# Kernel tuning notes

Measured on AMD Instinct MI355X. Metric: run time of the kernel, lower is better.

The kernel has to match this reference:

```python
import jax, jax.numpy as jnp
import numpy as np

B, T, N, D, H = 4, 8, 128, 256, 8
DH = D // H
SH_HID = 16
NUM_FEATS = 3
NUM_COEFF = 4  # l=0 (1) + l=1 (3)
Y0_CONST = 0.28209479177387814   # 1/(2*sqrt(pi)), e3nn 'integral' norm
Y1_CONST = 0.4886025119029199    # sqrt(3/(4*pi))


def setup_inputs() -> dict:
    key = jax.random.key(0)
    ks = jax.random.split(key, 16)
    rn = lambda k, shape, s=1.0: jax.random.normal(k, shape, dtype=jnp.float32) * s
    return {
        "x_0": rn(ks[0], (B, T, N, D)),
        "v_0": rn(ks[1], (B, T, N, D)),
        "concatenated_features": rn(ks[2], (B, T, N, D)),
        "q_data": rn(ks[3], (B, T, N, D)),
        "mask": jnp.ones((B, 1, N, 1), dtype=bool),
        "Wq": rn(ks[4], (D, D), 0.02), "bq": jnp.zeros((D,), jnp.float32),
        "Wkv": rn(ks[5], (NUM_FEATS, D, 2 * D), 0.02),
        "bkv": jnp.zeros((NUM_FEATS, 2 * D), jnp.float32),
        "Wo": rn(ks[6], (D, D), 0.02), "bo": jnp.zeros((D,), jnp.float32),
        "feature_weights": rn(ks[7], (NUM_FEATS,), 0.1),
        "attention_denom": jnp.full((H,), float(DH), dtype=jnp.float32),
        "sh_W1": rn(ks[8], (NUM_COEFF, SH_HID), 0.3), "sh_b1": jnp.zeros((SH_HID,), jnp.float32),
        "sh_W2": rn(ks[9], (SH_HID, SH_HID), 0.3), "sh_b2": jnp.zeros((SH_HID,), jnp.float32),
        "sh_W3": rn(ks[10], (SH_HID, H), 0.3), "sh_b3": jnp.zeros((H,), jnp.float32),
    }


def _rope(t, mask, T_, N_):
    # t: [B,H,S,dh]; time-only RoPE, groups of N_ nodes share a timestep. offset=0.
    B_, H_, S, dh = t.shape
    half = dh // 2
    freqs = 1.0 / (1000.0 ** (2.0 * jnp.arange(half, dtype=jnp.float32) / dh))  # [half]
    pos = jnp.repeat(jnp.arange(T_, dtype=jnp.float32), N_)  # [S]
    angle = pos[:, None] * freqs[None, :]  # [S, half]
    mask_seq = jnp.broadcast_to(mask, (B_, T_, N_, 1)).reshape(B_, 1, S, 1)
    cos_t = jnp.where(mask_seq, jnp.cos(angle)[None, None], 1.0)  # [B,1,S,half]
    sin_t = jnp.where(mask_seq, jnp.sin(angle)[None, None], 0.0)
    t1, t2 = t[..., 0::2], t[..., 1::2]
    return jnp.stack([t1 * cos_t - t2 * sin_t, t1 * sin_t + t2 * cos_t], axis=-1).reshape(t.shape)


def _sh_bias(coords, W1, b1, W2, b2, W3, b3):
    # coords: [B,S,3] -> bias [B,H,S,S]
    rel = coords[:, :, None, :] - coords[:, None, :, :]  # [B,S,S,3]
    norm = jnp.sqrt(jnp.sum(rel * rel, axis=-1, keepdims=True))
    u = rel / (norm + 1e-6)
    Y0 = jnp.full(u.shape[:-1] + (1,), Y0_CONST, dtype=u.dtype)
    Y1 = Y1_CONST * u[..., jnp.array([1, 2, 0])]  # e3nn l=1 order (y,z,x)
    sh = jnp.concatenate([Y0, Y1], axis=-1)  # [B,S,S,4]
    h = jax.nn.silu(sh @ W1 + b1)
    h = jax.nn.silu(h @ W2 + b2)
    bias = h @ W3 + b3  # [B,S,S,H]
    return jnp.transpose(bias, (0, 3, 1, 2))


def reference(x_0, v_0, concatenated_features, q_data, mask,
              Wq, bq, Wkv, bkv, Wo, bo, feature_weights, attention_denom,
              sh_W1, sh_b1, sh_W2, sh_b2, sh_W3, sh_b3):
    B_, T_, N_, D_ = q_data.shape
    S = T_ * N_
    H_ = attention_denom.shape[0]
    dh = D_ // H_

    q = (q_data.reshape(B_, S, D_) @ Wq + bq).reshape(B_, S, H_, dh).transpose(0, 2, 1, 3)
    q = _rope(q, mask, T_, N_)

    coords = x_0[..., :3].reshape(B_, S, 3)
    bias = _sh_bias(coords, sh_W1, sh_b1, sh_W2, sh_b2, sh_W3, sh_b3)  # [B,H,S,S]

    key_mask = jnp.broadcast_to(mask, (B_, T_, N_, 1)).reshape(B_, 1, 1, S)
    gates = jax.nn.softmax(feature_weights)

    out_sum = jnp.zeros_like(q)
    for i, feat in enumerate((x_0, v_0, concatenated_features)):
        kv = feat.reshape(B_, S, D_) @ Wkv[i] + bkv[i]  # [B,S,2D]
        k = kv[..., :D_].reshape(B_, S, H_, dh).transpose(0, 2, 1, 3)
        v = kv[..., D_:].reshape(B_, S, H_, dh).transpose(0, 2, 1, 3)
        k = _rope(k, mask, T_, N_)
        scores = jnp.einsum('bhqd,bhkd->bhqk', q, k) / attention_denom[None, :, None, None]
        scores = scores + bias
        scores = jnp.where(key_mask, scores, -1e9)
        attn = jax.nn.softmax(scores, axis=-1)
        out_sum = out_sum + gates[i] * jnp.einsum('bhqk,bhkd->bhqd', attn, v)

    out = out_sum.transpose(0, 2, 1, 3).reshape(B_, S, D_) @ Wo + bo  # [B,S,D]
    return out.reshape(B_ * T_, N_, D_)
```

## Files before the change

### kernel.cpp

```cpp
#include <hip/hip_runtime.h>
#include <hip/hip_bf16.h>
#include <math.h>


typedef __bf16 bf16;
typedef __attribute__((ext_vector_type(8))) __bf16 bf16x8;
typedef __attribute__((ext_vector_type(4))) __bf16 bf16x4;
typedef __attribute__((ext_vector_type(4))) float  f32x4;

#define MFMA16(a,b,c) __builtin_amdgcn_mfma_f32_16x16x32_bf16((a),(b),(c),0,0,0)
#define FRCP(x) __builtin_amdgcn_rcpf(x)

__global__ __launch_bounds__(256) void proj_kernel(
    const float* __restrict__ x0, const float* __restrict__ v0,
    const float* __restrict__ cf, const float* __restrict__ qd,
    const float* __restrict__ Wq, const float* __restrict__ bq,
    const float* __restrict__ Wkv, const float* __restrict__ bkv,
    const float* __restrict__ dn,
    bf16* __restrict__ Qb, bf16* __restrict__ Kb, bf16* __restrict__ Vtb)
{
  const int z  = blockIdx.z;
  const int mt = blockIdx.x;
  const int nt = blockIdx.y;
  if (z == 0 && nt >= 4) return;

  const float* A; const float* W; const float* bias; int ldw;
  if (z == 0){ A = qd; W = Wq; bias = bq; ldw = 256; }
  else {
    A = (z==1) ? x0 : (z==2) ? v0 : cf;
    W = Wkv + (size_t)(z-1)*256*512;
    bias = bkv + (size_t)(z-1)*512;
    ldw = 512;
  }

  __shared__ alignas(16) bf16 lds_a[64*264];
  __shared__ alignas(16) bf16 lds_w[64*264];
  const int t  = threadIdx.x;
  const int n0 = nt*64;

  #pragma unroll
  for (int i=0;i<16;i++){
    int flat = i*256 + t;
    int r = flat >> 6, c4 = flat & 63;
    float4 v = *(const float4*)(A + (size_t)(mt*64 + r)*256 + c4*4);
    bf16* dst = lds_a + r*264 + c4*4;
    dst[0]=(bf16)v.x; dst[1]=(bf16)v.y; dst[2]=(bf16)v.z; dst[3]=(bf16)v.w;
  }
  {
    int c4 = t & 15, kr = t >> 4;
    #pragma unroll
    for (int i=0;i<16;i++){
      int k = kr + i*16;
      float4 v = *(const float4*)(W + (size_t)k*ldw + n0 + c4*4);
      lds_w[(c4*4+0)*264 + k] = (bf16)v.x;
      lds_w[(c4*4+1)*264 + k] = (bf16)v.y;
      lds_w[(c4*4+2)*264 + k] = (bf16)v.z;
      lds_w[(c4*4+3)*264 + k] = (bf16)v.w;
    }
  }
  __syncthreads();

  const int w = t>>6, lane = t&63, lrow = lane&15, g = lane>>4;
  const f32x4 zf = {0.f,0.f,0.f,0.f};
  f32x4 acc[4] = {zf,zf,zf,zf};

  #pragma unroll
  for (int ks=0;ks<8;ks++){
    bf16x8 a = *(const bf16x8*)(lds_a + (w*16+lrow)*264 + ks*32 + g*8);
    #pragma unroll
    for (int n4=0;n4<4;n4++){
      bf16x8 bb = *(const bf16x8*)(lds_w + (n4*16+lrow)*264 + ks*32 + g*8);
      acc[n4] = MFMA16(a, bb, acc[n4]);
    }
  }

  #pragma unroll
  for (int n4=0;n4<4;n4++){
    int gcol = n0 + n4*16 + lrow;
    float bv = bias[gcol];
    if (z==0 || gcol < 256){
      int h = (gcol>>5)&7, d = gcol&31, j = d>>1;
      float freq = powf(1000.f, -(float)j*(1.f/16.f));
      float rs = (z==0) ? (1.f/dn[h]) : 1.f;
      #pragma unroll
      for (int rr=0;rr<4;rr++){
        int grow = mt*64 + w*16 + g*4 + rr;
        int bb = grow>>10, s = grow&1023;
        float v = acc[n4][rr] + bv;
        float p = __shfl_xor(v, 1);
        float ang = (float)(s>>7)*freq;
        float cs = cosf(ang), sn = sinf(ang);
        float o = (d&1) ? (p*sn + v*cs) : (v*cs - p*sn);
        o *= rs;
        bf16 ov = (bf16)o;
        if (z==0) Qb[((size_t)(bb*8+h)*1024 + s)*32 + d] = ov;
        else      Kb[((size_t)(((z-1)*4+bb)*8+h)*1024 + s)*32 + d] = ov;
      }
    } else {
      int hd = gcol - 256; int h = hd>>5, d = hd&31;
      int grow0 = mt*64 + w*16 + g*4;
      int bb = grow0>>10, s0 = grow0&1023;
      int s0p = (s0 & ~31) | (((s0>>2)&3)<<3) | (((s0>>4)&1)<<2);
      bf16x4 pk;
      #pragma unroll
      for (int rr=0;rr<4;rr++) pk[rr] = (bf16)(acc[n4][rr] + bv);
      *(bf16x4*)(Vtb + (((size_t)((z-1)*4+bb)*8 + h)*32 + d)*1024 + s0p) = pk;
    }
  }
}

__global__ __launch_bounds__(512) void attn_kernel(
    const bf16* __restrict__ Qb, const bf16* __restrict__ Kb, const bf16* __restrict__ Vtb,
    const float* __restrict__ x0, const float* __restrict__ fw,
    const float* __restrict__ W1, const float* __restrict__ b1,
    const float* __restrict__ W2, const float* __restrict__ b2,
    const float* __restrict__ W3, const float* __restrict__ b3,
    float* __restrict__ osum)
{
  const int bid = blockIdx.x;
  const int xcd = bid & 7;
  const int b   = xcd >> 1;
  const int qt  = (xcd & 1)*32 + (bid >> 3);
  const int q0  = qt*16;
  const int t = threadIdx.x, w = t>>6, lane = t&63, lrow = lane&15, g = lane>>4;

  __shared__ float ckA[1024][3];
  __shared__ float biasT[2][8*64*17];

  bf16x8 w1f, w2f, w3f;
  #pragma unroll
  for (int j=0;j<8;j++){
    w1f[j] = (g==0 && j<4)   ? (bf16)W1[j*16 + lrow]       : (bf16)0.f;
    w2f[j] = (j<4)           ? (bf16)W2[(4*g+j)*16 + lrow] : (bf16)0.f;
    w3f[j] = (j<4 && lrow<8) ? (bf16)W3[(4*g+j)*8 + lrow]  : (bf16)0.f;
  }
  float b1r[4], b2r[4], b3r[4];
  #pragma unroll
  for (int rr=0;rr<4;rr++){
    b1r[rr] = b1[g*4+rr];
    b2r[rr] = b2[g*4+rr];
    b3r[rr] = (g<2) ? b3[g*4+rr] : 0.f;
  }

  float f0=fw[0], f1=fw[1], f2=fw[2];
  float fm = fmaxf(f0, fmaxf(f1,f2));
  float e0=__expf(f0-fm), e1=__expf(f1-fm), e2=__expf(f2-fm);
  float ei = FRCP(e0+e1+e2);
  float gate[3] = {e0*ei, e1*ei, e2*ei};

  bf16x8 qf = *(const bf16x8*)(Qb + (((size_t)(b*8+w)*1024) + q0 + lrow)*32 + g*8);

  #pragma unroll
  for (int u=0;u<2;u++){
    int key = u*512 + t;
    const float* src = x0 + ((size_t)b*1024 + key)*256;
    ckA[key][0] = src[0]; ckA[key][1] = src[1]; ckA[key][2] = src[2];
  }
  __syncthreads();
  const float cqx = ckA[q0+lrow][0], cqy = ckA[q0+lrow][1], cqz = ckA[q0+lrow][2];

  float l_run[3] = {0.f,0.f,0.f};
  const f32x4 zf = {0.f,0.f,0.f,0.f};
  f32x4 acc[3][2];
  #pragma unroll
  for (int i=0;i<3;i++){ acc[i][0] = zf; acc[i][1] = zf; }

  for (int kt=0;kt<16;kt++){
    const int k0 = kt*64;
    float* bT = biasT[kt&1];

    #pragma unroll
    for (int m8=0;m8<8;m8++){
      const int m = w*8 + m8;
      float rx = cqx - ckA[k0+m][0];
      float ry = cqy - ckA[k0+m][1];
      float rz = cqz - ckA[k0+m][2];
      float inv = FRCP(__builtin_amdgcn_sqrtf(rx*rx+ry*ry+rz*rz) + 1e-6f);
      bf16x8 shf;
      #pragma unroll
      for (int j=0;j<8;j++) shf[j] = (bf16)0.f;
      if (g==0){
        shf[0] = (bf16)0.28209479177387814f;
        shf[1] = (bf16)(0.4886025119029199f*ry*inv);
        shf[2] = (bf16)(0.4886025119029199f*rz*inv);
        shf[3] = (bf16)(0.4886025119029199f*rx*inv);
      }
      f32x4 c1 = MFMA16(w1f, shf, zf);
      bf16x8 h1f;
      #pragma unroll
      for (int rr=0;rr<4;rr++){
        float hv = c1[rr] + b1r[rr];
        hv = hv * FRCP(1.f + __expf(-hv));
        bf16 hb = (bf16)hv;
        h1f[rr] = hb; h1f[rr+4] = hb;
      }
      f32x4 c2 = MFMA16(w2f, h1f, zf);
      bf16x8 h2f;
      #pragma unroll
      for (int rr=0;rr<4;rr++){
        float hv = c2[rr] + b2r[rr];
        hv = hv * FRCP(1.f + __expf(-hv));
        bf16 hb = (bf16)hv;
        h2f[rr] = hb; h2f[rr+4] = hb;
      }
      f32x4 c3 = MFMA16(w3f, h2f, zf);
      if (g < 2){
        #pragma unroll
        for (int rr=0;rr<4;rr++)
          bT[((g*4+rr)*64 + m)*17 + lrow] = c3[rr] + b3r[rr];
      }
    }
    __syncthreads();

    float bias_r[4][4];
    #pragma unroll
    for (int k16=0;k16<4;k16++)
      #pragma unroll
      for (int rr=0;rr<4;rr++)
        bias_r[k16][rr] = bT[(w*64 + k16*16 + g*4 + rr)*17 + lrow];

    #pragma unroll
    for (int i=0;i<3;i++){
      const bf16* Kbase = Kb + ((size_t)(i*4+b)*8 + w)*1024*32;
      float p[4][4];
      float ls = 0.f;
      #pragma unroll
      for (int k16=0;k16<4;k16++){
        bf16x8 kf = *(const bf16x8*)(Kbase + (size_t)(k0 + k16*16 + lrow)*32 + g*8);
        f32x4 sc = MFMA16(kf, qf, zf);
        #pragma unroll
        for (int rr=0;rr<4;rr++){
          float pv = __expf(sc[rr] + bias_r[k16][rr]);
          p[k16][rr] = pv;
          ls += pv;
        }
      }
      l_run[i] += ls;
      bf16x8 pf0, pf1;
      #pragma unroll
      for (int j=0;j<8;j++){
        pf0[j] = (bf16)p[(j>>2)][j&3];
        pf1[j] = (bf16)p[2+(j>>2)][j&3];
      }
      const bf16* Vbase = Vtb + ((size_t)(i*4+b)*8 + w)*32*1024;
      #pragma unroll
      for (int dt=0;dt<2;dt++){
        bf16x8 vf0 = *(const bf16x8*)(Vbase + (size_t)(dt*16+lrow)*1024 + k0      + g*8);
        bf16x8 vf1 = *(const bf16x8*)(Vbase + (size_t)(dt*16+lrow)*1024 + k0 + 32 + g*8);
        acc[i][dt] = MFMA16(vf0, pf0, acc[i][dt]);
        acc[i][dt] = MFMA16(vf1, pf1, acc[i][dt]);
      }
    }
  }

  float linv[3];
  #pragma unroll
  for (int i=0;i<3;i++){
    float l = l_run[i];
    l += __shfl_xor(l, 16);
    l += __shfl_xor(l, 32);
    linv[i] = gate[i]*FRCP(l);
  }
  #pragma unroll
  for (int dt=0;dt<2;dt++){
    f32x4 o;
    #pragma unroll
    for (int rr=0;rr<4;rr++)
      o[rr] = acc[0][dt][rr]*linv[0] + acc[1][dt][rr]*linv[1] + acc[2][dt][rr]*linv[2];
    *(f32x4*)(osum + ((size_t)b*1024 + q0 + lrow)*256 + w*32 + dt*16 + g*4) = o;
  }
}

__global__ __launch_bounds__(256) void oproj_kernel(
    const float* __restrict__ As, const float* __restrict__ Wo,
    const float* __restrict__ bo, float* __restrict__ out)
{
  const int mt = blockIdx.x, nt = blockIdx.y;
  __shared__ alignas(16) bf16 lds_a[64*264];
  __shared__ alignas(16) bf16 lds_w[64*264];
  const int t = threadIdx.x;
  const int n0 = nt*64;
  #pragma unroll
  for (int i=0;i<16;i++){
    int flat = i*256 + t;
    int r = flat >> 6, c4 = flat & 63;
    float4 v = *(const float4*)(As + (size_t)(mt*64 + r)*256 + c4*4);
    bf16* dst = lds_a + r*264 + c4*4;
    dst[0]=(bf16)v.x; dst[1]=(bf16)v.y; dst[2]=(bf16)v.z; dst[3]=(bf16)v.w;
  }
  {
    int c4 = t & 15, kr = t >> 4;
    #pragma unroll
    for (int i=0;i<16;i++){
      int k = kr + i*16;
      float4 v = *(const float4*)(Wo + (size_t)k*256 + n0 + c4*4);
      lds_w[(c4*4+0)*264 + k] = (bf16)v.x;
      lds_w[(c4*4+1)*264 + k] = (bf16)v.y;
      lds_w[(c4*4+2)*264 + k] = (bf16)v.z;
      lds_w[(c4*4+3)*264 + k] = (bf16)v.w;
    }
  }
  __syncthreads();
  const int w = t>>6, lane = t&63, lrow = lane&15, g = lane>>4;
  const f32x4 zf = {0.f,0.f,0.f,0.f};
  f32x4 acc[4] = {zf,zf,zf,zf};
  #pragma unroll
  for (int ks=0;ks<8;ks++){
    bf16x8 a = *(const bf16x8*)(lds_a + (w*16+lrow)*264 + ks*32 + g*8);
    #pragma unroll
    for (int n4=0;n4<4;n4++){
      bf16x8 bb = *(const bf16x8*)(lds_w + (n4*16+lrow)*264 + ks*32 + g*8);
      acc[n4] = MFMA16(a, bb, acc[n4]);
    }
  }
  #pragma unroll
  for (int n4=0;n4<4;n4++){
    int gcol = n0 + n4*16 + lrow;
    float bv = bo[gcol];
    #pragma unroll
    for (int rr=0;rr<4;rr++){
      int grow = mt*64 + w*16 + g*4 + rr;
      out[(size_t)grow*256 + gcol] = acc[n4][rr] + bv;
    }
  }
}

extern "C" void kernel_launch(void* const* d_in, const int* in_sizes, int n_in,
                              void* d_out, int out_size, void* d_ws, size_t ws_size,
                              hipStream_t stream)
{
  (void)in_sizes; (void)n_in; (void)out_size; (void)ws_size;
  const float* x0 = (const float*)d_in[0];
  const float* v0 = (const float*)d_in[1];
  const float* cf = (const float*)d_in[2];
  const float* qd = (const float*)d_in[3];
  const float* Wq = (const float*)d_in[5];
  const float* bq = (const float*)d_in[6];
  const float* Wkv= (const float*)d_in[7];
  const float* bkv= (const float*)d_in[8];
  const float* Wo = (const float*)d_in[9];
  const float* bo = (const float*)d_in[10];
  const float* fw = (const float*)d_in[11];
  const float* dn = (const float*)d_in[12];
  const float* W1 = (const float*)d_in[13];
  const float* b1 = (const float*)d_in[14];
  const float* W2 = (const float*)d_in[15];
  const float* b2 = (const float*)d_in[16];
  const float* W3 = (const float*)d_in[17];
  const float* b3 = (const float*)d_in[18];

  bf16*  Qb   = (bf16*)d_ws;
  bf16*  Kb   = Qb  + (size_t)4*8*1024*32;
  bf16*  Vtb  = Kb  + (size_t)3*4*8*1024*32;
  float* osum = (float*)(Vtb + (size_t)3*4*8*1024*32);
  float* outp = (float*)d_out;

  hipLaunchKernelGGL(proj_kernel, dim3(64,8,4), dim3(256), 0, stream,
                     x0, v0, cf, qd, Wq, bq, Wkv, bkv, dn, Qb, Kb, Vtb);
  hipLaunchKernelGGL(attn_kernel, dim3(256), dim3(512), 0, stream,
                     Qb, Kb, Vtb, x0, fw, W1,b1,W2,b2,W3,b3, osum);
  hipLaunchKernelGGL(oproj_kernel, dim3(64,4), dim3(256), 0, stream,
                     osum, Wo, bo, outp);
}
```

Measured before the change: 252.5 us.

## Split attention over key halves with combine kernel and vectorize RoPE stores

```diff
diff --git a/kernel.cpp b/kernel.cpp
--- a/kernel.cpp
+++ b/kernel.cpp
@@ -74,29 +74,50 @@
     }
   }
 
-  #pragma unroll
-  for (int n4=0;n4<4;n4++){
-    int gcol = n0 + n4*16 + lrow;
-    float bv = bias[gcol];
-    if (z==0 || gcol < 256){
-      int h = (gcol>>5)&7, d = gcol&31, j = d>>1;
-      float freq = powf(1000.f, -(float)j*(1.f/16.f));
-      float rs = (z==0) ? (1.f/dn[h]) : 1.f;
+  const bool isV = (z>0) && (nt>=4);
+  if (!isV){
+    const float tpos = (float)((mt & 15) >> 1);
+    const float Cln = 0.43172239f;
+    float fr_e = __expf(-Cln * (float)(lrow>>1));
+    float fr_o = __expf(-Cln * (float)(8 + (lrow>>1)));
+    float ae = tpos*fr_e, ao = tpos*fr_o;
+    float cs_e = __cosf(ae), sn_e = __sinf(ae);
+    float cs_o = __cosf(ao), sn_o = __sinf(ao);
+    float rs0 = 1.f, rs1 = 1.f;
+    if (z==0){ rs0 = 1.f/dn[(nt*2)&7]; rs1 = 1.f/dn[(nt*2+1)&7]; }
+
+    #pragma unroll
+    for (int n4=0;n4<4;n4++){
+      int gcol = n0 + n4*16 + lrow;
+      float bv = bias[gcol];
+      float cs = (n4&1)? cs_o : cs_e;
+      float sn = (n4&1)? sn_o : sn_e;
+      float rs = (n4>>1)? rs1 : rs0;
       #pragma unroll
       for (int rr=0;rr<4;rr++){
-        int grow = mt*64 + w*16 + g*4 + rr;
-        int bb = grow>>10, s = grow&1023;
         float v = acc[n4][rr] + bv;
         float p = __shfl_xor(v, 1);
-        float ang = (float)(s>>7)*freq;
-        float cs = cosf(ang), sn = sinf(ang);
-        float o = (d&1) ? (p*sn + v*cs) : (v*cs - p*sn);
+        float o = (lrow&1) ? (p*sn + v*cs) : (v*cs - p*sn);
         o *= rs;
-        bf16 ov = (bf16)o;
-        if (z==0) Qb[((size_t)(bb*8+h)*1024 + s)*32 + d] = ov;
-        else      Kb[((size_t)(((z-1)*4+bb)*8+h)*1024 + s)*32 + d] = ov;
-      }
-    } else {
+        lds_a[(w*16 + g*4 + rr)*264 + n4*16 + lrow] = (bf16)o;
+      }
+    }
+    int row = lane>>2, c8 = lane&3;
+    int srow = mt*64 + w*16 + row;
+    int bb = srow>>10, s = srow&1023;
+    #pragma unroll
+    for (int hh=0; hh<2; hh++){
+      bf16x8 val = *(const bf16x8*)(lds_a + (w*16+row)*264 + hh*32 + c8*8);
+      int h = (nt*2 + hh)&7;
+      bf16* dst = (z==0) ? (Qb + ((size_t)(bb*8+h)*1024 + s)*32 + c8*8)
+                         : (Kb + ((size_t)(((z-1)*4+bb)*8+h)*1024 + s)*32 + c8*8);
+      *(bf16x8*)dst = val;
+    }
+  } else {
+    #pragma unroll
+    for (int n4=0;n4<4;n4++){
+      int gcol = n0 + n4*16 + lrow;
+      float bv = bias[gcol];
       int hd = gcol - 256; int h = hd>>5, d = hd&31;
       int grow0 = mt*64 + w*16 + g*4;
       int bb = grow0>>10, s0 = grow0&1023;
@@ -109,23 +130,29 @@
   }
 }
 
+template<bool PART>
 __global__ __launch_bounds__(512) void attn_kernel(
     const bf16* __restrict__ Qb, const bf16* __restrict__ Kb, const bf16* __restrict__ Vtb,
     const float* __restrict__ x0, const float* __restrict__ fw,
     const float* __restrict__ W1, const float* __restrict__ b1,
     const float* __restrict__ W2, const float* __restrict__ b2,
     const float* __restrict__ W3, const float* __restrict__ b3,
-    float* __restrict__ osum)
+    float* __restrict__ osum, float* __restrict__ Pp, float* __restrict__ Lp)
 {
   const int bid = blockIdx.x;
   const int xcd = bid & 7;
   const int b   = xcd >> 1;
-  const int qt  = (xcd & 1)*32 + (bid >> 3);
-  const int q0  = qt*16;
+  int qt, split;
+  if (PART){ int r = bid>>3; qt = (xcd&1)*32 + (r&31); split = r>>5; }
+  else     { qt = (xcd&1)*32 + (bid>>3); split = 0; }
+  const int q0 = qt*16;
+  constexpr int KTS = PART ? 8 : 16;
+  constexpr int KC  = PART ? 512 : 1024;
+  const int kbase = split*512;
   const int t = threadIdx.x, w = t>>6, lane = t&63, lrow = lane&15, g = lane>>4;
 
-  __shared__ float ckA[1024][3];
-  __shared__ float biasT[2][8*64*17];
+  __shared__ float ckA[KC][3];
+  __shared__ float biasT[8*64*17];
 
   bf16x8 w1f, w2f, w3f;
   #pragma unroll
@@ -142,22 +169,17 @@
     b3r[rr] = (g<2) ? b3[g*4+rr] : 0.f;
   }
 
-  float f0=fw[0], f1=fw[1], f2=fw[2];
-  float fm = fmaxf(f0, fmaxf(f1,f2));
-  float e0=__expf(f0-fm), e1=__expf(f1-fm), e2=__expf(f2-fm);
-  float ei = FRCP(e0+e1+e2);
-  float gate[3] = {e0*ei, e1*ei, e2*ei};
-
   bf16x8 qf = *(const bf16x8*)(Qb + (((size_t)(b*8+w)*1024) + q0 + lrow)*32 + g*8);
 
   #pragma unroll
-  for (int u=0;u<2;u++){
+  for (int u=0; u<KC/512; u++){
     int key = u*512 + t;
-    const float* src = x0 + ((size_t)b*1024 + key)*256;
+    const float* src = x0 + ((size_t)b*1024 + kbase + key)*256;
     ckA[key][0] = src[0]; ckA[key][1] = src[1]; ckA[key][2] = src[2];
   }
+  const float* qsrc = x0 + ((size_t)b*1024 + q0 + lrow)*256;
+  const float cqx = qsrc[0], cqy = qsrc[1], cqz = qsrc[2];
   __syncthreads();
-  const float cqx = ckA[q0+lrow][0], cqy = ckA[q0+lrow][1], cqz = ckA[q0+lrow][2];
 
   float l_run[3] = {0.f,0.f,0.f};
   const f32x4 zf = {0.f,0.f,0.f,0.f};
@@ -165,9 +187,9 @@
   #pragma unroll
   for (int i=0;i<3;i++){ acc[i][0] = zf; acc[i][1] = zf; }
 
-  for (int kt=0;kt<16;kt++){
+  for (int kt=0;kt<KTS;kt++){
     const int k0 = kt*64;
-    float* bT = biasT[kt&1];
+    const int kg = kbase + k0;
 
     #pragma unroll
     for (int m8=0;m8<8;m8++){
@@ -207,7 +229,7 @@
       if (g < 2){
         #pragma unroll
         for (int rr=0;rr<4;rr++)
-          bT[((g*4+rr)*64 + m)*17 + lrow] = c3[rr] + b3r[rr];
+          biasT[((g*4+rr)*64 + m)*17 + lrow] = c3[rr] + b3r[rr];
       }
     }
     __syncthreads();
@@ -217,7 +239,7 @@
     for (int k16=0;k16<4;k16++)
       #pragma unroll
       for (int rr=0;rr<4;rr++)
-        bias_r[k16][rr] = bT[(w*64 + k16*16 + g*4 + rr)*17 + lrow];
+        bias_r[k16][rr] = biasT[(w*64 + k16*16 + g*4 + rr)*17 + lrow];
 
     #pragma unroll
     for (int i=0;i<3;i++){
@@ -226,7 +248,7 @@
       float ls = 0.f;
       #pragma unroll
       for (int k16=0;k16<4;k16++){
-        bf16x8 kf = *(const bf16x8*)(Kbase + (size_t)(k0 + k16*16 + lrow)*32 + g*8);
+        bf16x8 kf = *(const bf16x8*)(Kbase + (size_t)(kg + k16*16 + lrow)*32 + g*8);
         f32x4 sc = MFMA16(kf, qf, zf);
         #pragma unroll
         for (int rr=0;rr<4;rr++){
@@ -245,30 +267,79 @@
       const bf16* Vbase = Vtb + ((size_t)(i*4+b)*8 + w)*32*1024;
       #pragma unroll
       for (int dt=0;dt<2;dt++){
-        bf16x8 vf0 = *(const bf16x8*)(Vbase + (size_t)(dt*16+lrow)*1024 + k0      + g*8);
-        bf16x8 vf1 = *(const bf16x8*)(Vbase + (size_t)(dt*16+lrow)*1024 + k0 + 32 + g*8);
+        bf16x8 vf0 = *(const bf16x8*)(Vbase + (size_t)(dt*16+lrow)*1024 + kg      + g*8);
+        bf16x8 vf1 = *(const bf16x8*)(Vbase + (size_t)(dt*16+lrow)*1024 + kg + 32 + g*8);
         acc[i][dt] = MFMA16(vf0, pf0, acc[i][dt]);
         acc[i][dt] = MFMA16(vf1, pf1, acc[i][dt]);
       }
     }
-  }
-
-  float linv[3];
+    __syncthreads();
+  }
+
+  if (PART){
+    #pragma unroll
+    for (int i=0;i<3;i++){
+      float l = l_run[i];
+      l += __shfl_xor(l, 16);
+      l += __shfl_xor(l, 32);
+      if (lane < 16)
+        Lp[((size_t)(i*2+split)*4+b)*8192 + w*1024 + q0 + lrow] = l;
+      #pragma unroll
+      for (int dt=0;dt<2;dt++)
+        *(f32x4*)(Pp + (((size_t)(i*2+split)*4 + b)*1024 + q0 + lrow)*256
+                     + w*32 + dt*16 + g*4) = acc[i][dt];
+    }
+  } else {
+    float f0=fw[0], f1=fw[1], f2=fw[2];
+    float fm = fmaxf(f0, fmaxf(f1,f2));
+    float e0=__expf(f0-fm), e1=__expf(f1-fm), e2=__expf(f2-fm);
+    float ei = FRCP(e0+e1+e2);
+    float gate[3] = {e0*ei, e1*ei, e2*ei};
+    float linv[3];
+    #pragma unroll
+    for (int i=0;i<3;i++){
+      float l = l_run[i];
+      l += __shfl_xor(l, 16);
+      l += __shfl_xor(l, 32);
+      linv[i] = gate[i]*FRCP(l);
+    }
+    #pragma unroll
+    for (int dt=0;dt<2;dt++){
+      f32x4 o;
+      #pragma unroll
+      for (int rr=0;rr<4;rr++)
+        o[rr] = acc[0][dt][rr]*linv[0] + acc[1][dt][rr]*linv[1] + acc[2][dt][rr]*linv[2];
+      *(f32x4*)(osum + ((size_t)b*1024 + q0 + lrow)*256 + w*32 + dt*16 + g*4) = o;
+    }
+  }
+}
+
+__global__ __launch_bounds__(256) void combine_kernel(
+    const float* __restrict__ Pp, const float* __restrict__ Lp,
+    const float* __restrict__ fw, float* __restrict__ osum)
+{
+  int idx  = blockIdx.x*256 + threadIdx.x;
+  int col4 = idx & 63;
+  int row  = idx >> 6;
+  int b = row >> 10, q = row & 1023;
+  int h = col4 >> 3;
+  float f0=fw[0], f1=fw[1], f2=fw[2];
+  float fm = fmaxf(f0, fmaxf(f1,f2));
+  float e0=__expf(f0-fm), e1=__expf(f1-fm), e2=__expf(f2-fm);
+  float ei = 1.f/(e0+e1+e2);
+  float gate[3] = {e0*ei, e1*ei, e2*ei};
+  f32x4 o = {0.f,0.f,0.f,0.f};
   #pragma unroll
   for (int i=0;i<3;i++){
-    float l = l_run[i];
-    l += __shfl_xor(l, 16);
-    l += __shfl_xor(l, 32);
-    linv[i] = gate[i]*FRCP(l);
-  }
-  #pragma unroll
-  for (int dt=0;dt<2;dt++){
-    f32x4 o;
-    #pragma unroll
-    for (int rr=0;rr<4;rr++)
-      o[rr] = acc[0][dt][rr]*linv[0] + acc[1][dt][rr]*linv[1] + acc[2][dt][rr]*linv[2];
-    *(f32x4*)(osum + ((size_t)b*1024 + q0 + lrow)*256 + w*32 + dt*16 + g*4) = o;
-  }
+    f32x4 a = ((const f32x4*)Pp)[(((size_t)(i*2+0)*4 + b)*1024 + q)*64 + col4];
+    f32x4 c = ((const f32x4*)Pp)[(((size_t)(i*2+1)*4 + b)*1024 + q)*64 + col4];
+    float l = Lp[((size_t)(i*2+0)*4+b)*8192 + h*1024 + q]
+            + Lp[((size_t)(i*2+1)*4+b)*8192 + h*1024 + q];
+    float s = gate[i]/l;
+    #pragma unroll
+    for (int rr=0;rr<4;rr++) o[rr] += (a[rr]+c[rr])*s;
+  }
+  ((f32x4*)osum)[idx] = o;
 }
 
 __global__ __launch_bounds__(256) void oproj_kernel(
@@ -329,7 +400,7 @@
                               void* d_out, int out_size, void* d_ws, size_t ws_size,
                               hipStream_t stream)
 {
-  (void)in_sizes; (void)n_in; (void)out_size; (void)ws_size;
+  (void)in_sizes; (void)n_in; (void)out_size;
   const float* x0 = (const float*)d_in[0];
   const float* v0 = (const float*)d_in[1];
   const float* cf = (const float*)d_in[2];
@@ -349,16 +420,29 @@
   const float* W3 = (const float*)d_in[17];
   const float* b3 = (const float*)d_in[18];
 
+  const size_t nQ = (size_t)4*8*1024*32;
+  const size_t nK = (size_t)3*4*8*1024*32;
   bf16*  Qb   = (bf16*)d_ws;
-  bf16*  Kb   = Qb  + (size_t)4*8*1024*32;
-  bf16*  Vtb  = Kb  + (size_t)3*4*8*1024*32;
-  float* osum = (float*)(Vtb + (size_t)3*4*8*1024*32);
+  bf16*  Kb   = Qb + nQ;
+  bf16*  Vtb  = Kb + nK;
+  float* osum = (float*)(Vtb + nK);
+  float* Pp   = osum + (size_t)4*1024*256;
+  float* Lp   = Pp + (size_t)3*2*4*1024*256;
+  const size_t need_part = (nQ + 2*nK)*2
+                         + ((size_t)4*1024*256 + (size_t)3*2*4*1024*256 + (size_t)3*2*4*8*1024)*4;
   float* outp = (float*)d_out;
 
   hipLaunchKernelGGL(proj_kernel, dim3(64,8,4), dim3(256), 0, stream,
                      x0, v0, cf, qd, Wq, bq, Wkv, bkv, dn, Qb, Kb, Vtb);
-  hipLaunchKernelGGL(attn_kernel, dim3(256), dim3(512), 0, stream,
-                     Qb, Kb, Vtb, x0, fw, W1,b1,W2,b2,W3,b3, osum);
+  if (ws_size >= need_part){
+    hipLaunchKernelGGL((attn_kernel<true>), dim3(512), dim3(512), 0, stream,
+                       Qb, Kb, Vtb, x0, fw, W1,b1,W2,b2,W3,b3, osum, Pp, Lp);
+    hipLaunchKernelGGL(combine_kernel, dim3(1024), dim3(256), 0, stream,
+                       Pp, Lp, fw, osum);
+  } else {
+    hipLaunchKernelGGL((attn_kernel<false>), dim3(256), dim3(512), 0, stream,
+                       Qb, Kb, Vtb, x0, fw, W1,b1,W2,b2,W3,b3, osum, Pp, Lp);
+  }
   hipLaunchKernelGGL(oproj_kernel, dim3(64,4), dim3(256), 0, stream,
                      osum, Wo, bo, outp);
 }
```

Result: slower. 260.3 us (+3.1%).
